# Kernel optimization log

Measured on AMD Instinct MI355X. Metric: run time of the kernel, lower is better.

## Reference

```python
import jax, jax.numpy as jnp
import numpy as np

N = 50000          # nodes
E = 1_600_000      # edges (avg degree 32)
F_IN = 128         # num_node_features
HID = 128          # hidden_dim
G = 512            # graphs in batch
NEG_SLOPE = 0.2    # PyG GATConv default


def setup_inputs() -> dict:
    key = jax.random.key(0)
    ks = jax.random.split(key, 13)
    s_in = 1.0 / np.sqrt(F_IN)
    s_h = 1.0 / np.sqrt(HID)
    return {
        "x": jax.random.normal(ks[0], (N, F_IN), jnp.float32),
        "edge_index": jax.random.randint(ks[1], (2, E), 0, N, dtype=jnp.int32),
        "batch": jnp.sort(jax.random.randint(ks[2], (N,), 0, G, dtype=jnp.int32)),
        "W1": jax.random.normal(ks[3], (F_IN, HID), jnp.float32) * s_in,
        "a_src1": jax.random.normal(ks[4], (HID,), jnp.float32) * s_h,
        "a_dst1": jax.random.normal(ks[5], (HID,), jnp.float32) * s_h,
        "b1": jnp.zeros((HID,), jnp.float32),
        "W2": jax.random.normal(ks[6], (HID, HID), jnp.float32) * s_h,
        "a_src2": jax.random.normal(ks[7], (HID,), jnp.float32) * s_h,
        "a_dst2": jax.random.normal(ks[8], (HID,), jnp.float32) * s_h,
        "b2": jnp.zeros((HID,), jnp.float32),
        "fc_w": jax.random.normal(ks[9], (2 * HID, 1), jnp.float32) * (1.0 / np.sqrt(2 * HID)),
        "fc_b": jnp.zeros((1,), jnp.float32),
    }


def _gat_conv(x, W, a_src, a_dst, b, src, dst, n):
    # PyG GATConv, heads=1: h = xW; alpha_e = softmax_dst(leaky_relu(a_s.h[src] + a_d.h[dst]))
    h = x @ W                                    # [N, C]
    asrc = h @ a_src                             # [N]
    adst = h @ a_dst                             # [N]
    logits = jax.nn.leaky_relu(asrc[src] + adst[dst], NEG_SLOPE)  # [E']
    m = jax.ops.segment_max(logits, dst, num_segments=n)
    ex = jnp.exp(logits - m[dst])
    denom = jax.ops.segment_sum(ex, dst, num_segments=n)
    alpha = ex / denom[dst]                      # segment softmax over incoming edges
    out = jax.ops.segment_sum(h[src] * alpha[:, None], dst, num_segments=n)
    return out + b


def reference(x, edge_index, batch, W1, a_src1, a_dst1, b1, W2, a_src2, a_dst2, b2, fc_w, fc_b):
    n = x.shape[0]
    loop = jnp.arange(n, dtype=edge_index.dtype)   # add_self_loops=True (PyG default)
    src = jnp.concatenate([edge_index[0], loop])
    dst = jnp.concatenate([edge_index[1], loop])

    h = jax.nn.relu(x)
    h = jax.nn.relu(_gat_conv(h, W1, a_src1, a_dst1, b1, src, dst, n))
    h = jax.nn.relu(_gat_conv(h, W2, a_src2, a_dst2, b2, src, dst, n))

    counts = jax.ops.segment_sum(jnp.ones((n,), h.dtype), batch, num_segments=G)
    maxp = jax.ops.segment_max(h, batch, num_segments=G)
    maxp = jnp.where(counts[:, None] > 0, maxp, 0.0)
    meanp = jax.ops.segment_sum(h, batch, num_segments=G) / jnp.maximum(counts, 1.0)[:, None]
    pooled = jnp.concatenate([maxp, meanp], axis=1)  # [G, 2*HID]
    return pooled @ fc_w + fc_b                      # [G, 1]
```

## Files before the change

### kernel.cpp

```cpp
#include <hip/hip_runtime.h>
#include <math.h>


#define LEAKY 0.2f
#define CAP 128

__device__ __forceinline__ unsigned short f2bf(float x) {
    unsigned int u = __float_as_uint(x);
    unsigned int r = (u + 0x7FFFu + ((u >> 16) & 1u)) >> 16;
    return (unsigned short)r;
}
__device__ __forceinline__ float bf2f(unsigned short b) {
    return __uint_as_float((unsigned int)b << 16);
}

__global__ __launch_bounds__(256) void scatterx(const int* __restrict__ ei,
                                                int* __restrict__ cnt,
                                                unsigned short* __restrict__ col,
                                                int E, int N) {
    const int g = blockIdx.x & 7;
    const int chunk = blockIdx.x >> 3;
    const int lo = (int)(((long long)N * g) >> 3);
    const int hi = (int)(((long long)N * (g + 1)) >> 3);
    const int base = chunk * 4096;
    int fin = base + 4096; if (fin > E) fin = E;
    for (int i = base + threadIdx.x; i < fin; i += 256) {
        int d = ei[E + i];
        if (d >= lo && d < hi) {
            int s = ei[i];
            int pos = atomicAdd(&cnt[d], 1);
            if (pos < CAP) col[(size_t)d * CAP + pos] = (unsigned short)s;
        }
    }
}

__global__ __launch_bounds__(256) void gemm64(const float* __restrict__ A,
                                              const float* __restrict__ B,
                                              float* __restrict__ C,
                                              unsigned short* __restrict__ Cb,
                                              const float* __restrict__ a_src,
                                              const float* __restrict__ a_dst,
                                              float* __restrict__ asv,
                                              float* __restrict__ adv,
                                              int n, int applyRelu) {
    __shared__ float Ast[32][68];
    __shared__ float Bs[32][132];
    __shared__ float sredS[64][17];
    __shared__ float sredD[64][17];
    const int tid = threadIdx.x;
    const int row0 = blockIdx.x * 64;
    const int tx = tid & 15;
    const int ty = tid >> 4;
    float acc[4][8] = {};

    for (int k0 = 0; k0 < 128; k0 += 32) {
        {
            int kv = tid & 7, r = tid >> 3;
            int kk = kv * 4;
#pragma unroll
            for (int i = 0; i < 2; ++i) {
                int rr = r + 32 * i;
                int grow = row0 + rr;
                float4 v = make_float4(0.f, 0.f, 0.f, 0.f);
                if (grow < n) {
                    v = *(const float4*)(A + (size_t)grow * 128 + k0 + kk);
                    if (applyRelu) {
                        v.x = fmaxf(v.x, 0.f); v.y = fmaxf(v.y, 0.f);
                        v.z = fmaxf(v.z, 0.f); v.w = fmaxf(v.w, 0.f);
                    }
                }
                Ast[kk + 0][rr] = v.x;
                Ast[kk + 1][rr] = v.y;
                Ast[kk + 2][rr] = v.z;
                Ast[kk + 3][rr] = v.w;
            }
        }
        {
            int cv = tid & 31, kr = tid >> 5;
#pragma unroll
            for (int i = 0; i < 4; ++i) {
                int kk2 = kr + 8 * i;
                float4 v = *(const float4*)(B + (size_t)(k0 + kk2) * 128 + cv * 4);
                Bs[kk2][cv * 4 + 0] = v.x; Bs[kk2][cv * 4 + 1] = v.y;
                Bs[kk2][cv * 4 + 2] = v.z; Bs[kk2][cv * 4 + 3] = v.w;
            }
        }
        __syncthreads();
#pragma unroll
        for (int k = 0; k < 32; ++k) {
            float4 a4 = *(const float4*)&Ast[k][ty * 4];
            float4 q0 = *(const float4*)&Bs[k][tx * 8];
            float4 q1 = *(const float4*)&Bs[k][tx * 8 + 4];
            float a[4] = { a4.x, a4.y, a4.z, a4.w };
            float b[8] = { q0.x, q0.y, q0.z, q0.w, q1.x, q1.y, q1.z, q1.w };
#pragma unroll
            for (int i = 0; i < 4; ++i)
#pragma unroll
                for (int j = 0; j < 8; ++j) acc[i][j] += a[i] * b[j];
        }
        __syncthreads();
    }

    float asl[8], adl[8];
#pragma unroll
    for (int j = 0; j < 8; ++j) {
        asl[j] = a_src[tx * 8 + j];
        adl[j] = a_dst[tx * 8 + j];
    }
#pragma unroll
    for (int i = 0; i < 4; ++i) {
        int rr = ty * 4 + i;
        int grow = row0 + rr;
        float ps = 0.f, pd = 0.f;
#pragma unroll
        for (int j = 0; j < 8; ++j) {
            ps += acc[i][j] * asl[j];
            pd += acc[i][j] * adl[j];
        }
        sredS[rr][tx] = ps;
        sredD[rr][tx] = pd;
        if (grow < n) {
            float4* dst = (float4*)(C + (size_t)grow * 128 + tx * 8);
            dst[0] = make_float4(acc[i][0], acc[i][1], acc[i][2], acc[i][3]);
            dst[1] = make_float4(acc[i][4], acc[i][5], acc[i][6], acc[i][7]);
            uint4 pk;
            pk.x = (unsigned)f2bf(acc[i][0]) | ((unsigned)f2bf(acc[i][1]) << 16);
            pk.y = (unsigned)f2bf(acc[i][2]) | ((unsigned)f2bf(acc[i][3]) << 16);
            pk.z = (unsigned)f2bf(acc[i][4]) | ((unsigned)f2bf(acc[i][5]) << 16);
            pk.w = (unsigned)f2bf(acc[i][6]) | ((unsigned)f2bf(acc[i][7]) << 16);
            *(uint4*)(Cb + (size_t)grow * 128 + tx * 8) = pk;
        }
    }
    __syncthreads();
    if (tid < 64) {
        int grow = row0 + tid;
        if (grow < n) {
            float ps = 0.f, pd = 0.f;
#pragma unroll
            for (int j = 0; j < 16; ++j) {
                ps += sredS[tid][j];
                pd += sredD[tid][j];
            }
            asv[grow] = ps;
            adv[grow] = pd;
        }
    }
}

__global__ __launch_bounds__(256) void aggregate(const unsigned short* __restrict__ hb,
                                                 const int* __restrict__ cnt,
                                                 const unsigned short* __restrict__ col,
                                                 const float* __restrict__ asv,
                                                 const float* __restrict__ adv,
                                                 const float* __restrict__ bias,
                                                 float* __restrict__ out, int n) {
    __shared__ int   scol[4][128];
    __shared__ float swt[4][128];
    const int wv = threadIdx.x >> 6;
    const int lane = threadIdx.x & 63;
    const int w = blockIdx.x * 4 + wv;
    if (w >= n) return;
    int deg = cnt[w];
    if (deg > CAP - 1) deg = CAP - 1;
    const int D = deg + 1;
    const size_t start = (size_t)w * CAP;
    const float ad = adv[w];

    int c0 = 0, c1 = 0;
    float l0 = -INFINITY, l1 = -INFINITY;
    if (lane < D) {
        c0 = (lane < deg) ? (int)col[start + lane] : w;
        l0 = asv[c0] + ad;
        l0 = l0 > 0.f ? l0 : LEAKY * l0;
    }
    if (64 + lane < D) {
        c1 = (64 + lane < deg) ? (int)col[start + 64 + lane] : w;
        l1 = asv[c1] + ad;
        l1 = l1 > 0.f ? l1 : LEAKY * l1;
    }
    float m = fmaxf(l0, l1);
#pragma unroll
    for (int off = 32; off; off >>= 1) m = fmaxf(m, __shfl_xor(m, off, 64));
    float e0 = (lane < D) ? __expf(l0 - m) : 0.f;
    float e1 = (64 + lane < D) ? __expf(l1 - m) : 0.f;
    float s = e0 + e1;
#pragma unroll
    for (int off = 32; off; off >>= 1) s += __shfl_xor(s, off, 64);
    float inv = 1.f / s;
    if (lane < D)      { scol[wv][lane] = c0;      swt[wv][lane] = e0; }
    if (64 + lane < D) { scol[wv][64 + lane] = c1; swt[wv][64 + lane] = e1; }

    const int hw = lane >> 5;
    const int sl = lane & 31;
    float4 aa[8];
#pragma unroll
    for (int j = 0; j < 8; ++j) aa[j] = make_float4(0.f, 0.f, 0.f, 0.f);
    for (int i = 0; i < D; i += 16) {
        int cs[8]; float ws[8];
#pragma unroll
        for (int j = 0; j < 8; ++j) {
            int idx = i + 2 * j + hw;
            int cl = idx < D ? idx : D - 1;
            cs[j] = scol[wv][cl];
            ws[j] = (idx < D) ? swt[wv][idx] : 0.f;
        }
        ushort4 rs[8];
#pragma unroll
        for (int j = 0; j < 8; ++j)
            rs[j] = *((const ushort4*)(hb + (size_t)cs[j] * 128) + sl);
#pragma unroll
        for (int j = 0; j < 8; ++j) {
            aa[j].x += ws[j] * bf2f(rs[j].x);
            aa[j].y += ws[j] * bf2f(rs[j].y);
            aa[j].z += ws[j] * bf2f(rs[j].z);
            aa[j].w += ws[j] * bf2f(rs[j].w);
        }
    }
#pragma unroll
    for (int j = 1; j < 8; ++j) {
        aa[0].x += aa[j].x; aa[0].y += aa[j].y;
        aa[0].z += aa[j].z; aa[0].w += aa[j].w;
    }
    aa[0].x += __shfl_xor(aa[0].x, 32);
    aa[0].y += __shfl_xor(aa[0].y, 32);
    aa[0].z += __shfl_xor(aa[0].z, 32);
    aa[0].w += __shfl_xor(aa[0].w, 32);
    if (hw == 0) {
        float4 b = ((const float4*)bias)[sl];
        float4 o;
        o.x = fmaxf(aa[0].x * inv + b.x, 0.f);
        o.y = fmaxf(aa[0].y * inv + b.y, 0.f);
        o.z = fmaxf(aa[0].z * inv + b.z, 0.f);
        o.w = fmaxf(aa[0].w * inv + b.w, 0.f);
        *((float4*)(out + (size_t)w * 128) + sl) = o;
    }
}

__global__ __launch_bounds__(128) void poolfc(const float* __restrict__ h2,
                                              const int* __restrict__ batch,
                                              const float* __restrict__ fcw,
                                              const float* __restrict__ fcb,
                                              float* __restrict__ out, int G, int n) {
    __shared__ int seg[2];
    int g = blockIdx.x;
    int f = threadIdx.x;
    if (f < 2) {
        int target = g + f;
        int lo = 0, hi = n;
        while (lo < hi) {
            int mid = (lo + hi) >> 1;
            if (batch[mid] < target) lo = mid + 1; else hi = mid;
        }
        seg[f] = lo;
    }
    __syncthreads();
    int s = seg[0], e = seg[1];
    float m = -INFINITY, sum = 0.f;
    for (int node = s; node < e; ++node) {
        float v = h2[(size_t)node * 128 + f];
        m = fmaxf(m, v);
        sum += v;
    }
    int cnt = e - s;
    float maxp = (cnt > 0) ? m : 0.f;
    float cden = (float)(cnt > 0 ? cnt : 1);
    float meanp = sum / cden;
    float p = maxp * fcw[f] + meanp * fcw[128 + f];
    __shared__ float red[128];
    red[f] = p;
    __syncthreads();
    for (int off = 64; off; off >>= 1) {
        if (f < off) red[f] += red[f + off];
        __syncthreads();
    }
    if (f == 0) out[g] = red[0] + fcb[0];
}

extern "C" void kernel_launch(void* const* d_in, const int* in_sizes, int n_in,
                              void* d_out, int out_size, void* d_ws, size_t ws_size,
                              hipStream_t stream) {
    const int N = in_sizes[0] / 128;
    const int E = in_sizes[1] / 2;
    const int G = out_size;

    const float* x      = (const float*)d_in[0];
    const int*   ei     = (const int*)d_in[1];
    const int*   batch  = (const int*)d_in[2];
    const float* W1     = (const float*)d_in[3];
    const float* a_src1 = (const float*)d_in[4];
    const float* a_dst1 = (const float*)d_in[5];
    const float* b1     = (const float*)d_in[6];
    const float* W2     = (const float*)d_in[7];
    const float* a_src2 = (const float*)d_in[8];
    const float* a_dst2 = (const float*)d_in[9];
    const float* b2     = (const float*)d_in[10];
    const float* fcw    = (const float*)d_in[11];
    const float* fcb    = (const float*)d_in[12];
    float* out = (float*)d_out;

    char* wp = (char*)d_ws;
    auto alloc = [&](size_t bytes) -> void* {
        void* p = (void*)wp;
        wp += (bytes + 255) & ~(size_t)255;
        return p;
    };
    int* cnt     = (int*)alloc(sizeof(int) * N);
    unsigned short* col = (unsigned short*)alloc(sizeof(unsigned short) * (size_t)N * CAP);
    float* hp    = (float*)alloc(sizeof(float) * (size_t)N * 128);
    float* ha    = (float*)alloc(sizeof(float) * (size_t)N * 128);
    unsigned short* hb = (unsigned short*)alloc(sizeof(unsigned short) * (size_t)N * 128);
    float* asv   = (float*)alloc(sizeof(float) * N);
    float* adv   = (float*)alloc(sizeof(float) * N);

    hipMemsetAsync(cnt, 0, sizeof(int) * N, stream);

    const int gemmGrid = (N + 63) / 64;
    const int waveGrid = (N + 3) / 4;
    const int nchunk = (E + 4095) / 4096;

    scatterx<<<nchunk * 8, 256, 0, stream>>>(ei, cnt, col, E, N);

    gemm64<<<gemmGrid, 256, 0, stream>>>(x, W1, hp, hb, a_src1, a_dst1, asv, adv, N, 1);
    aggregate<<<waveGrid, 256, 0, stream>>>(hb, cnt, col, asv, adv, b1, ha, N);

    gemm64<<<gemmGrid, 256, 0, stream>>>(ha, W2, hp, hb, a_src2, a_dst2, asv, adv, N, 0);
    aggregate<<<waveGrid, 256, 0, stream>>>(hb, cnt, col, asv, adv, b2, ha, N);

    poolfc<<<G, 128, 0, stream>>>(ha, batch, fcw, fcb, out, G, N);
}
```

Before: 391.6 us.

## Make edge scatter XCC-aware with per-range work queues

The CSR-building scatter kernel now reads the hardware XCC id and has each block first pull chunks from the destination-range queue matching its XCC, then steal from the other ranges. The goal is to keep atomics and column writes for a node range local to one XCC's L2 and to balance the load dynamically through a persistent grid of 2048 blocks. In exchange it adds a global atomic and two block barriers per chunk, plus an extra memset for the queue counters.

```diff
diff --git a/kernel.cpp b/kernel.cpp
--- a/kernel.cpp
+++ b/kernel.cpp
@@ -14,22 +14,35 @@
     return __uint_as_float((unsigned int)b << 16);
 }
 
-__global__ __launch_bounds__(256) void scatterx(const int* __restrict__ ei,
+__global__ __launch_bounds__(256) void scatterq(const int* __restrict__ ei,
                                                 int* __restrict__ cnt,
                                                 unsigned short* __restrict__ col,
-                                                int E, int N) {
-    const int g = blockIdx.x & 7;
-    const int chunk = blockIdx.x >> 3;
-    const int lo = (int)(((long long)N * g) >> 3);
-    const int hi = (int)(((long long)N * (g + 1)) >> 3);
-    const int base = chunk * 4096;
-    int fin = base + 4096; if (fin > E) fin = E;
-    for (int i = base + threadIdx.x; i < fin; i += 256) {
-        int d = ei[E + i];
-        if (d >= lo && d < hi) {
-            int s = ei[i];
-            int pos = atomicAdd(&cnt[d], 1);
-            if (pos < CAP) col[(size_t)d * CAP + pos] = (unsigned short)s;
+                                                int* __restrict__ queues,
+                                                int E, int N, int nchunk) {
+    __shared__ int sChunk;
+    unsigned xcc = 0;
+    asm("s_getreg_b32 %0, hwreg(HW_REG_XCC_ID)" : "=s"(xcc));
+    const int myr = (int)(xcc & 7u);
+    for (int t = 0; t < 8; ++t) {
+        const int r = (myr + t) & 7;
+        const int lo = (int)(((long long)N * r) >> 3);
+        const int hi = (int)(((long long)N * (r + 1)) >> 3);
+        for (;;) {
+            if (threadIdx.x == 0) sChunk = atomicAdd(&queues[r], 1);
+            __syncthreads();
+            const int c = sChunk;
+            __syncthreads();
+            if (c >= nchunk) break;
+            const int base = c * 4096;
+            int fin = base + 4096; if (fin > E) fin = E;
+            for (int i = base + threadIdx.x; i < fin; i += 256) {
+                int d = ei[E + i];
+                if (d >= lo && d < hi) {
+                    int s = ei[i];
+                    int pos = atomicAdd(&cnt[d], 1);
+                    if (pos < CAP) col[(size_t)d * CAP + pos] = (unsigned short)s;
+                }
+            }
         }
     }
 }
@@ -305,6 +318,7 @@
         return p;
     };
     int* cnt     = (int*)alloc(sizeof(int) * N);
+    int* queues  = (int*)alloc(sizeof(int) * 8);
     unsigned short* col = (unsigned short*)alloc(sizeof(unsigned short) * (size_t)N * CAP);
     float* hp    = (float*)alloc(sizeof(float) * (size_t)N * 128);
     float* ha    = (float*)alloc(sizeof(float) * (size_t)N * 128);
@@ -313,12 +327,13 @@
     float* adv   = (float*)alloc(sizeof(float) * N);
 
     hipMemsetAsync(cnt, 0, sizeof(int) * N, stream);
+    hipMemsetAsync(queues, 0, sizeof(int) * 8, stream);
 
     const int gemmGrid = (N + 63) / 64;
     const int waveGrid = (N + 3) / 4;
     const int nchunk = (E + 4095) / 4096;
 
-    scatterx<<<nchunk * 8, 256, 0, stream>>>(ei, cnt, col, E, N);
+    scatterq<<<2048, 256, 0, stream>>>(ei, cnt, col, queues, E, N, nchunk);
 
     gemm64<<<gemmGrid, 256, 0, stream>>>(x, W1, hp, hb, a_src1, a_dst1, asv, adv, N, 1);
     aggregate<<<waveGrid, 256, 0, stream>>>(hb, cnt, col, asv, adv, b1, ha, N);
```

After: 585.4 us. 49.5% more time.

## Replace per-node atomic scatter with two-pass XCC-local binning into node-group cells

Applied to the files above, without the earlier changes.

The single scatter kernel, which reads the edge list eight times and does global atomics per destination node, becomes a two-pass build. The first pass bins packed (dst,src) pairs into 64-node cells, partitioned by the XCC that runs the block so atomics stay on that die. The second pass builds the per-node column lists with shared-memory atomics. This cuts repeated edge reads and contended global atomics, at the cost of an extra intermediate buffer and a fixed cell capacity of 512. That capacity could drop edges if one XCC's share for a cell exceeds it, and the 16-bit packing assumes node ids fit in 16 bits.

```diff
diff --git a/kernel.cpp b/kernel.cpp
--- a/kernel.cpp
+++ b/kernel.cpp
@@ -4,6 +4,7 @@
 
 #define LEAKY 0.2f
 #define CAP 128
+#define CELLCAP 512
 
 __device__ __forceinline__ unsigned short f2bf(float x) {
     unsigned int u = __float_as_uint(x);
@@ -14,24 +15,50 @@
     return __uint_as_float((unsigned int)b << 16);
 }
 
-__global__ __launch_bounds__(256) void scatterx(const int* __restrict__ ei,
-                                                int* __restrict__ cnt,
-                                                unsigned short* __restrict__ col,
-                                                int E, int N) {
-    const int g = blockIdx.x & 7;
-    const int chunk = blockIdx.x >> 3;
-    const int lo = (int)(((long long)N * g) >> 3);
-    const int hi = (int)(((long long)N * (g + 1)) >> 3);
-    const int base = chunk * 4096;
-    int fin = base + 4096; if (fin > E) fin = E;
+__global__ __launch_bounds__(256) void binA(const int* __restrict__ ei,
+                                            int* __restrict__ ccur,
+                                            unsigned int* __restrict__ pairs,
+                                            int E, int NB) {
+    unsigned xcc = 0;
+    asm("s_getreg_b32 %0, hwreg(HW_REG_XCC_ID)" : "=s"(xcc));
+    const int xbase = (int)(xcc & 7u) * NB;
+    const int base = blockIdx.x * 1024;
+    int fin = base + 1024; if (fin > E) fin = E;
     for (int i = base + threadIdx.x; i < fin; i += 256) {
+        int s = ei[i];
         int d = ei[E + i];
-        if (d >= lo && d < hi) {
-            int s = ei[i];
-            int pos = atomicAdd(&cnt[d], 1);
+        int cell = xbase + (d >> 6);
+        int pos = atomicAdd(&ccur[cell], 1);
+        if (pos < CELLCAP)
+            pairs[(size_t)cell * CELLCAP + pos] = ((unsigned)d << 16) | (unsigned)s;
+    }
+}
+
+__global__ __launch_bounds__(256) void binB(const unsigned int* __restrict__ pairs,
+                                            const int* __restrict__ ccur,
+                                            int* __restrict__ cnt,
+                                            unsigned short* __restrict__ col,
+                                            int N, int NB) {
+    __shared__ int cur[64];
+    const int b = blockIdx.x;
+    const int n0 = b * 64;
+    const int t = threadIdx.x;
+    if (t < 64) cur[t] = 0;
+    __syncthreads();
+    for (int x = 0; x < 8; ++x) {
+        const int cell = x * NB + b;
+        int len = ccur[cell]; if (len > CELLCAP) len = CELLCAP;
+        const unsigned int* seg = pairs + (size_t)cell * CELLCAP;
+        for (int i = t; i < len; i += 256) {
+            unsigned p = seg[i];
+            int d = (int)(p >> 16);
+            int s = (int)(p & 0xFFFFu);
+            int pos = atomicAdd(&cur[d - n0], 1);
             if (pos < CAP) col[(size_t)d * CAP + pos] = (unsigned short)s;
         }
     }
+    __syncthreads();
+    if (t < 64 && n0 + t < N) cnt[n0 + t] = cur[t];
 }
 
 __global__ __launch_bounds__(256) void gemm64(const float* __restrict__ A,
@@ -282,6 +309,7 @@
     const int N = in_sizes[0] / 128;
     const int E = in_sizes[1] / 2;
     const int G = out_size;
+    const int NB = (N + 63) / 64;
 
     const float* x      = (const float*)d_in[0];
     const int*   ei     = (const int*)d_in[1];
@@ -305,6 +333,8 @@
         return p;
     };
     int* cnt     = (int*)alloc(sizeof(int) * N);
+    int* ccur    = (int*)alloc(sizeof(int) * 8 * NB);
+    unsigned int* pairs = (unsigned int*)alloc(sizeof(unsigned int) * (size_t)8 * NB * CELLCAP);
     unsigned short* col = (unsigned short*)alloc(sizeof(unsigned short) * (size_t)N * CAP);
     float* hp    = (float*)alloc(sizeof(float) * (size_t)N * 128);
     float* ha    = (float*)alloc(sizeof(float) * (size_t)N * 128);
@@ -312,13 +342,13 @@
     float* asv   = (float*)alloc(sizeof(float) * N);
     float* adv   = (float*)alloc(sizeof(float) * N);
 
-    hipMemsetAsync(cnt, 0, sizeof(int) * N, stream);
+    hipMemsetAsync(ccur, 0, sizeof(int) * 8 * NB, stream);
 
     const int gemmGrid = (N + 63) / 64;
     const int waveGrid = (N + 3) / 4;
-    const int nchunk = (E + 4095) / 4096;
-
-    scatterx<<<nchunk * 8, 256, 0, stream>>>(ei, cnt, col, E, N);
+
+    binA<<<(E + 1023) / 1024, 256, 0, stream>>>(ei, ccur, pairs, E, NB);
+    binB<<<NB, 256, 0, stream>>>(pairs, ccur, cnt, col, N, NB);
 
     gemm64<<<gemmGrid, 256, 0, stream>>>(x, W1, hp, hb, a_src1, a_dst1, asv, adv, N, 1);
     aggregate<<<waveGrid, 256, 0, stream>>>(hb, cnt, col, asv, adv, b1, ha, N);
```

Result: slower. 417.9 us (+6.7%).
